# Performance work log

Measured on AMD Instinct MI355X. Metric: run time of the kernel, lower is better.

The kernel has to match this reference:

```python
import jax, jax.numpy as jnp
import numpy as np
from jax import lax

EPS = 1e-6
B, C, F, K = 64, 512, 1024, 3

def rmsnorm2d(x, w):
    # normalize over channel dim (axis=1), learnable per-channel scale
    inv = lax.rsqrt(jnp.mean(x * x, axis=1, keepdims=True) + EPS)
    return x * inv * w[None, :, None, None]

def pointwise(x, W, b):
    # 1x1 conv == per-pixel matmul: [B,C,H,F] x [O,C] -> [B,O,H,F]
    return jnp.einsum('bchf,oc->bohf', x, W) + b[None, :, None, None]

def depthwise_band(x, W, b):
    # depthwise conv, kernel (1,K), same padding along freq axis
    y = lax.conv_general_dilated(
        x, W,
        window_strides=(1, 1),
        padding=((0, 0), (K // 2, K // 2)),
        dimension_numbers=('NCHW', 'OIHW', 'NCHW'),
        feature_group_count=C)
    return y + b[None, :, None, None]

def setup_inputs() -> dict:
    key = jax.random.key(0)
    ks = jax.random.split(key, 6)
    s = 0.02
    return {
        'x_t': jax.random.normal(ks[0], (B, C, 1, F), jnp.float32),
        'h_prev': jax.random.normal(ks[1], (B, C, 1, F), jnp.float32),
        'in_norm_w': jnp.ones((C,), jnp.float32),
        'hid_norm_w': jnp.ones((C,), jnp.float32),
        'out_norm_w': jnp.ones((C,), jnp.float32),
        'xW': jax.random.normal(ks[2], (3 * C, C), jnp.float32) * s,
        'xb': jnp.zeros((3 * C,), jnp.float32),
        'hmixW': jax.random.normal(ks[3], (C, 1, 1, K), jnp.float32) * s,
        'hmixb': jnp.zeros((C,), jnp.float32),
        'hW': jax.random.normal(ks[4], (3 * C, C), jnp.float32) * s,
        'hb': jnp.zeros((3 * C,), jnp.float32),
    }

def reference(x_t, h_prev, in_norm_w, hid_norm_w, out_norm_w,
              xW, xb, hmixW, hmixb, hW, hb):
    xg = pointwise(rmsnorm2d(x_t, in_norm_w), xW, xb)            # [B,3C,1,F]
    hg = pointwise(depthwise_band(rmsnorm2d(h_prev, hid_norm_w), hmixW, hmixb), hW, hb)
    xr, xz, xn = jnp.split(xg, 3, axis=1)
    hr, hz, hn = jnp.split(hg, 3, axis=1)
    reset = jax.nn.sigmoid(xr + hr)
    update = jax.nn.sigmoid(xz + hz)
    cand = jnp.tanh(xn + reset * hn)
    h_new = (1.0 - update) * cand + update * h_prev
    return rmsnorm2d(h_new + x_t, out_norm_w)
```

## Files before the change

### kernel.cpp

```cpp
#include <hip/hip_runtime.h>

typedef __attribute__((ext_vector_type(8))) short short8;
typedef __attribute__((ext_vector_type(4))) float f32x4;
typedef __attribute__((ext_vector_type(4))) unsigned short u16x4;
typedef unsigned short u16;
typedef unsigned int u32;

#define EPSV 1e-6f

__device__ __forceinline__ u16 f2bf(float f){
  u32 u = __float_as_uint(f);
  u = u + 0x7fffu + ((u >> 16) & 1u);
  return (u16)(u >> 16);
}
__device__ __forceinline__ float bf2f(u16 h){
  return __uint_as_float(((u32)h) << 16);
}
__device__ __forceinline__ float sigm(float v){ return 1.f/(1.f + __expf(-v)); }
__device__ __forceinline__ float tanh_fast(float g){
  float e = __expf(-2.f*fabsf(g));
  return copysignf((1.f - e)/(1.f + e), g);
}
__device__ __forceinline__ void gload_lds16(const void* g, void* l){
  __builtin_amdgcn_global_load_lds(
      (const __attribute__((address_space(1))) u32*)g,
      (__attribute__((address_space(3))) u32*)l, 16, 0, 0);
}

#define WS_WXB   0u
#define WS_WHB   1572864u
#define WS_CB    3145728u
#define WS_SSQP  3153920u
#define WS_SBF   7348224u
#define WS_NEED  74457088u

#define GG_SMEM  147456

extern "C" __global__ void wprep(const float* __restrict__ xW, const float* __restrict__ hW,
                                 const float* __restrict__ inw, const float* __restrict__ hidw,
                                 const float* __restrict__ xb, const float* __restrict__ hmixb,
                                 const float* __restrict__ hb,
                                 u16* __restrict__ xWb, u16* __restrict__ hWb,
                                 float* __restrict__ cb){
  __shared__ float red[4];
  const int n = blockIdx.x;
  const int tid = threadIdx.x;
  float pb = 0.f;
  for (int k = tid; k < 512; k += 256){
    float xw = xW[n*512 + k], hw = hW[n*512 + k];
    xWb[n*512 + k] = f2bf(xw * inw[k]);
    hWb[n*512 + k] = f2bf(hw * hidw[k]);
    pb += hw * hmixb[k];
  }
  #pragma unroll
  for (int off = 1; off < 64; off <<= 1) pb += __shfl_xor(pb, off);
  if ((tid & 63) == 0) red[tid >> 6] = pb;
  __syncthreads();
  if (tid == 0){
    float dot = red[0] + red[1] + red[2] + red[3];
    if (n < 1024){ cb[n] = xb[n] + hb[n] + dot; }
    else         { cb[n] = xb[n]; cb[n + 512] = hb[n] + dot; }
  }
}

extern "C" __global__ void __launch_bounds__(256)
wbuild(const float* __restrict__ x, const float* __restrict__ h,
       const float* __restrict__ hmixW,
       u16* __restrict__ Ax, u16* __restrict__ Ahm)
{
  __shared__ float tile[32][264];
  __shared__ float invx_s[256];
  __shared__ float invh_s[258];
  __shared__ float hmw_s[1536];

  const int b = blockIdx.y, fc = blockIdx.x;
  const int f0 = fc*256;
  const int t = threadIdx.x;
  const int r = t >> 3, q = t & 7;

  for (int i = t; i < 1536; i += 256) hmw_s[i] = hmixW[i];

  float ssq = 0.f;
  for (int cc = 0; cc < 16; ++cc){
    __syncthreads();
    const float* src = x + ((size_t)(b*512 + cc*32 + r))*1024 + f0;
    #pragma unroll
    for (int i = 0; i < 8; ++i)
      *(f32x4*)&tile[r][q*4 + i*32] = *(const f32x4*)(src + q*4 + i*32);
    __syncthreads();
    float p = 0.f;
    #pragma unroll
    for (int rr = 0; rr < 32; ++rr){ float v = tile[rr][t]; p += v*v; }
    ssq += p;
  }
  invx_s[t] = rsqrtf(ssq*(1.f/512.f) + EPSV);
  for (int cc = 0; cc < 16; ++cc){
    __syncthreads();
    const float* src = x + ((size_t)(b*512 + cc*32 + r))*1024 + f0;
    #pragma unroll
    for (int i = 0; i < 8; ++i)
      *(f32x4*)&tile[r][q*4 + i*32] = *(const f32x4*)(src + q*4 + i*32);
    __syncthreads();
    #pragma unroll
    for (int it = 0; it < 4; ++it){
      int id = it*256 + t;
      int pix = id >> 2, c8 = (id & 3)*8;
      float iv = invx_s[pix];
      short8 pk;
      #pragma unroll
      for (int j = 0; j < 8; ++j) pk[j] = (short)f2bf(tile[c8+j][pix]*iv);
      *(short8*)(Ax + ((size_t)(b*1024 + f0 + pix))*512 + cc*32 + c8) = pk;
    }
  }
  float ssqh = 0.f, ssqL = 0.f, ssqR = 0.f;
  for (int cc = 0; cc < 16; ++cc){
    __syncthreads();
    const float* src = h + ((size_t)(b*512 + cc*32 + r))*1024 + f0;
    #pragma unroll
    for (int i = 0; i < 8; ++i)
      *(f32x4*)&tile[r][q*4 + i*32] = *(const f32x4*)(src + q*4 + i*32);
    if (t < 32){
      tile[t][256] = (f0 > 0) ? h[((size_t)(b*512 + cc*32 + t))*1024 + f0 - 1] : 0.f;
    } else if (t < 64){
      int rr = t - 32;
      tile[rr][257] = (f0 + 256 < 1024) ? h[((size_t)(b*512 + cc*32 + rr))*1024 + f0 + 256] : 0.f;
    }
    __syncthreads();
    float p = 0.f;
    #pragma unroll
    for (int rr = 0; rr < 32; ++rr){ float v = tile[rr][t]; p += v*v; }
    ssqh += p;
    if (t == 0){ float p2=0.f; for (int rr=0; rr<32; ++rr){ float v=tile[rr][256]; p2+=v*v; } ssqL += p2; }
    if (t == 1){ float p2=0.f; for (int rr=0; rr<32; ++rr){ float v=tile[rr][257]; p2+=v*v; } ssqR += p2; }
  }
  invh_s[1 + t] = rsqrtf(ssqh*(1.f/512.f) + EPSV);
  if (t == 0) invh_s[0]   = rsqrtf(ssqL*(1.f/512.f) + EPSV);
  if (t == 1) invh_s[257] = rsqrtf(ssqR*(1.f/512.f) + EPSV);
  for (int cc = 0; cc < 16; ++cc){
    __syncthreads();
    const float* src = h + ((size_t)(b*512 + cc*32 + r))*1024 + f0;
    #pragma unroll
    for (int i = 0; i < 8; ++i)
      *(f32x4*)&tile[r][q*4 + i*32] = *(const f32x4*)(src + q*4 + i*32);
    if (t < 32){
      tile[t][256] = (f0 > 0) ? h[((size_t)(b*512 + cc*32 + t))*1024 + f0 - 1] : 0.f;
    } else if (t < 64){
      int rr = t - 32;
      tile[rr][257] = (f0 + 256 < 1024) ? h[((size_t)(b*512 + cc*32 + rr))*1024 + f0 + 256] : 0.f;
    }
    __syncthreads();
    #pragma unroll
    for (int it = 0; it < 4; ++it){
      int id = it*256 + t;
      int pix = id >> 2, c8 = (id & 3)*8;
      int colL = (pix == 0)   ? 256 : (pix - 1);
      int colR = (pix == 255) ? 257 : (pix + 1);
      float iL = invh_s[pix], iC = invh_s[pix+1], iR = invh_s[pix+2];
      short8 pk;
      #pragma unroll
      for (int j = 0; j < 8; ++j){
        int c = c8 + j;
        int cg = cc*32 + c;
        float v = hmw_s[cg*3+0]*tile[c][colL]*iL
                + hmw_s[cg*3+1]*tile[c][pix ]*iC
                + hmw_s[cg*3+2]*tile[c][colR]*iR;
        pk[j] = (short)f2bf(v);
      }
      *(short8*)(Ahm + ((size_t)(b*1024 + f0 + pix))*512 + cc*32 + c8) = pk;
    }
  }
}

extern "C" __global__ void __launch_bounds__(256, 1)
gemm_gates(const float* __restrict__ x, const float* __restrict__ h,
           const u16* __restrict__ Abase,
           const u16* __restrict__ xWb, const u16* __restrict__ hWb,
           const float* __restrict__ cb,
           float* __restrict__ ssqp, u16* __restrict__ sbf)
{
  extern __shared__ __align__(16) char smem[];
  const int t = threadIdx.x;
  const int bid = blockIdx.x;
  const int swz = (bid & 7)*512 + (bid >> 3);
  const int mh = swz >> 4, ch = swz & 15;
  const int b = mh >> 2, f0 = (mh & 3)*256;
  const int c0 = ch*32;
  const int pixbase = b*1024 + f0;
  const int w = t >> 6, lane = t & 63, li = lane & 15, lg = lane >> 4;

  char* Bbase = smem + 49152;

  int rrA[4], kqA[4];
  #pragma unroll
  for (int uu = 0; uu < 4; ++uu){
    int u = w*256 + uu*64 + lane;
    rrA[uu] = ((u >> 5) & 7)*8 + (u & 7) + w*64;
    kqA[uu] = (u >> 3) & 3;
  }

  auto stageB = [&](const u16* Wsrc){
    #pragma unroll
    for (int i = 0; i < 24; ++i){
      int fi = i*4 + w;
      int kk = fi / 6, rem = fi - kk*6;
      int g = rem >> 1, ct = rem & 1;
      const u16* src = Wsrc + ((size_t)(g*512 + c0 + ct*16 + li))*512 + kk*32 + lg*8;
      gload_lds16(src, Bbase + fi*1024);
    }
  };
  auto stageA = [&](const u16* Asrc, int kk, int buf){
    char* adst = smem + buf*16384 + w*4096;
    #pragma unroll
    for (int uu = 0; uu < 4; ++uu){
      gload_lds16(Asrc + ((size_t)(pixbase + rrA[uu]))*512 + kk*32 + kqA[uu]*8,
                  adst + uu*1024);
    }
  };

  f32x4 accr[2][4] = {}, accz[2][4] = {}, accg1[2][4] = {}, accg2[2][4] = {};

  auto kstep = [&](int kk, int buf, f32x4 (&accg)[2][4]){
    const char* ab = smem + buf*16384 + w*4096;
    short8 af[4];
    #pragma unroll
    for (int mf = 0; mf < 4; ++mf){
      int rl = mf*16 + li;
      af[mf] = *(const short8*)(ab + ((rl >> 3) << 9) + (lg << 7) + ((rl & 7) << 4));
    }
    #pragma unroll
    for (int ct = 0; ct < 2; ++ct){
      const char* bb = Bbase + (kk*6 + ct)*1024 + lane*16;
      short8 bf0 = *(const short8*)(bb);
      short8 bf1 = *(const short8*)(bb + 2048);
      short8 bf2 = *(const short8*)(bb + 4096);
      #pragma unroll
      for (int mf = 0; mf < 4; ++mf){
        accr[ct][mf] = __builtin_amdgcn_mfma_f32_16x16x32_bf16(af[mf], bf0, accr[ct][mf], 0,0,0);
        accz[ct][mf] = __builtin_amdgcn_mfma_f32_16x16x32_bf16(af[mf], bf1, accz[ct][mf], 0,0,0);
        accg[ct][mf] = __builtin_amdgcn_mfma_f32_16x16x32_bf16(af[mf], bf2, accg[ct][mf], 0,0,0);
      }
    }
  };

  stageB(xWb);
  stageA(Abase, 0, 0);
  stageA(Abase, 1, 1);
  __syncthreads();
  #pragma unroll
  for (int j = 0; j < 16; ++j){
    if (j < 14) stageA(Abase, j + 2, (j + 2) % 3);
    kstep(j, j % 3, accg1);
    if (j < 14)      { asm volatile("s_waitcnt vmcnt(4)" ::: "memory"); }
    else if (j == 14){ asm volatile("s_waitcnt vmcnt(0)" ::: "memory"); }
    __builtin_amdgcn_sched_barrier(0);
  }
  __syncthreads();
  const u16* A1 = Abase + 33554432;
  stageB(hWb);
  stageA(A1, 0, 0);
  stageA(A1, 1, 1);
  __syncthreads();
  #pragma unroll
  for (int j = 0; j < 16; ++j){
    if (j < 14) stageA(A1, j + 2, (j + 2) % 3);
    kstep(j, j % 3, accg2);
    if (j < 14)      { asm volatile("s_waitcnt vmcnt(4)" ::: "memory"); }
    else if (j == 14){ asm volatile("s_waitcnt vmcnt(0)" ::: "memory"); }
    __builtin_amdgcn_sched_barrier(0);
  }
  __syncthreads();

  float (*stg)[264] = (float(*)[264])smem;
  float ps[4][4] = {};
  #pragma unroll
  for (int ct = 0; ct < 2; ++ct){
    const int c = c0 + ct*16 + li;
    const float cbr = cb[c], cbz = cb[512 + c], xbn = cb[1024 + c], hbn = cb[1536 + c];
    #pragma unroll
    for (int mf = 0; mf < 4; ++mf){
      const int f = f0 + w*64 + mf*16 + lg*4;
      const size_t gidx = ((size_t)(b*512 + c))*1024 + f;
      f32x4 hp = *(const f32x4*)(h + gidx);
      f32x4 xt = *(const f32x4*)(x + gidx);
      f32x4 sv;
      #pragma unroll
      for (int j = 0; j < 4; ++j){
        float rr = sigm(accr[ct][mf][j] + cbr);
        float zz = sigm(accz[ct][mf][j] + cbz);
        float g  = accg1[ct][mf][j] + xbn + rr*(accg2[ct][mf][j] + hbn);
        float th = tanh_fast(g);
        float s  = (1.f - zz)*th + zz*hp[j] + xt[j];
        sv[j] = s;
        ps[mf][j] += s*s;
      }
      *(f32x4*)&stg[ct*16 + li][w*64 + mf*16 + lg*4] = sv;
    }
  }
  #pragma unroll
  for (int off = 1; off < 16; off <<= 1)
    #pragma unroll
    for (int mf = 0; mf < 4; ++mf)
      #pragma unroll
      for (int j = 0; j < 4; ++j)
        ps[mf][j] += __shfl_xor(ps[mf][j], off);
  if (li == 0){
    #pragma unroll
    for (int mf = 0; mf < 4; ++mf){
      f32x4 v; v[0]=ps[mf][0]; v[1]=ps[mf][1]; v[2]=ps[mf][2]; v[3]=ps[mf][3];
      *(f32x4*)(ssqp + (size_t)ch*65536 + pixbase + w*64 + mf*16 + lg*4) = v;
    }
  }
  __syncthreads();
  {
    const int cl = t >> 3, seg = t & 7;
    u16* dst = sbf + ((size_t)(b*512 + c0 + cl))*1024 + f0 + seg*32;
    #pragma unroll
    for (int qq = 0; qq < 2; ++qq){
      f32x4 a0 = *(const f32x4*)&stg[cl][seg*32 + qq*16 + 0];
      f32x4 a1 = *(const f32x4*)&stg[cl][seg*32 + qq*16 + 4];
      f32x4 a2 = *(const f32x4*)&stg[cl][seg*32 + qq*16 + 8];
      f32x4 a3 = *(const f32x4*)&stg[cl][seg*32 + qq*16 + 12];
      short8 p0, p1;
      #pragma unroll
      for (int j = 0; j < 4; ++j){
        p0[j]   = (short)f2bf(a0[j]); p0[j+4] = (short)f2bf(a1[j]);
        p1[j]   = (short)f2bf(a2[j]); p1[j+4] = (short)f2bf(a3[j]);
      }
      *(short8*)(dst + qq*16)     = p0;
      *(short8*)(dst + qq*16 + 8) = p1;
    }
  }
}

extern "C" __global__ void __launch_bounds__(256)
outnorm(const float* __restrict__ ssqp, const u16* __restrict__ sbf,
        const float* __restrict__ outw, float* __restrict__ out)
{
  __shared__ float invf[1024];
  const int b = blockIdx.y, cch = blockIdx.x;
  const int t = threadIdx.x;
  f32x4 acc = {};
  #pragma unroll
  for (int p = 0; p < 16; ++p){
    f32x4 v = *(const f32x4*)(ssqp + (size_t)p*65536 + b*1024 + t*4);
    acc[0]+=v[0]; acc[1]+=v[1]; acc[2]+=v[2]; acc[3]+=v[3];
  }
  f32x4 iv;
  #pragma unroll
  for (int j = 0; j < 4; ++j) iv[j] = rsqrtf(acc[j]*(1.f/512.f) + EPSV);
  *(f32x4*)&invf[t*4] = iv;
  __syncthreads();
  for (int cl = 0; cl < 32; ++cl){
    const int c = cch*32 + cl;
    const float ow = outw[c];
    const u16* row = sbf + ((size_t)(b*512 + c))*1024;
    u16x4 sv = *(const u16x4*)(row + t*4);
    f32x4 o;
    #pragma unroll
    for (int j = 0; j < 4; ++j) o[j] = bf2f(sv[j]) * invf[t*4 + j] * ow;
    *(f32x4*)(out + ((size_t)(b*512 + c))*1024 + t*4) = o;
  }
}

#define FB_AXN_OFF 0
#define FB_AHM_OFF 32768
#define FB_RAW_OFF 65536
#define FB_PART_OFF 102400
#define FB_INVX_OFF 104512
#define FB_INVH_OFF 104640
#define FB_SSQ2_OFF 104784
#define FB_INVO_OFF 105936
#define FB_SMEM_BYTES 106112

extern "C" __global__ void fb_wconv(const float* __restrict__ xW, const float* __restrict__ hW,
                                    u16* __restrict__ xWb, u16* __restrict__ hWb){
  int i = blockIdx.x*256 + threadIdx.x;
  xWb[i] = f2bf(xW[i]);
  hWb[i] = f2bf(hW[i]);
}

extern "C" __global__ void __launch_bounds__(512, 2)
fb_gru(const float* __restrict__ x, const float* __restrict__ h,
       const float* __restrict__ inw, const float* __restrict__ hidw,
       const float* __restrict__ outw,
       const float* __restrict__ xb, const float* __restrict__ hmixWc,
       const float* __restrict__ hmixb, const float* __restrict__ hb,
       const u16* __restrict__ xWb, const u16* __restrict__ hWb,
       float* __restrict__ out)
{
  extern __shared__ __align__(16) char smem[];
  const int b  = blockIdx.y;
  const int f0 = blockIdx.x * 32;
  const int t  = threadIdx.x;
  u16* raw = (u16*)(smem + FB_RAW_OFF);
  float* part = (float*)(smem + FB_PART_OFF);
  {
    const int fq = t & 7, cb2 = t >> 3;
    #pragma unroll
    for (int pass = 0; pass < 8; ++pass){
      int c = pass*64 + cb2;
      f32x4 v = *(const f32x4*)(x + ((size_t)(b*512 + c))*1024 + f0 + fq*4);
      u16* d = raw + c*36 + fq*4;
      d[0] = f2bf(v[0]); d[1] = f2bf(v[1]); d[2] = f2bf(v[2]); d[3] = f2bf(v[3]);
    }
  }
  __syncthreads();
  {
    const int f = t & 31, cs = t >> 5;
    float p = 0.f;
    for (int i = 0; i < 32; ++i){ float v = bf2f(raw[(cs*32 + i)*36 + f]); p += v*v; }
    part[cs*33 + f] = p;
  }
  __syncthreads();
  if (t < 32){
    float s = 0.f;
    for (int i = 0; i < 16; ++i) s += part[i*33 + t];
    ((float*)(smem + FB_INVX_OFF))[t] = rsqrtf(s*(1.f/512.f) + EPSV);
  }
  __syncthreads();
  {
    const int f = t >> 4, cc = t & 15;
    const float iv = ((float*)(smem + FB_INVX_OFF))[f];
    #pragma unroll
    for (int it = 0; it < 4; ++it){
      int cbase = (cc + it*16)*8;
      short8 pk;
      #pragma unroll
      for (int j = 0; j < 8; ++j){
        float v = bf2f(raw[(cbase+j)*36 + f]) * iv * inw[cbase+j];
        pk[j] = (short)f2bf(v);
      }
      *(short8*)(smem + FB_AXN_OFF + f*1024 + ((cbase*2) ^ ((f&7)<<4))) = pk;
    }
  }
  __syncthreads();
  {
    const int fq = t & 7, cb2 = t >> 3;
    #pragma unroll
    for (int pass = 0; pass < 8; ++pass){
      int c = pass*64 + cb2;
      f32x4 v = *(const f32x4*)(h + ((size_t)(b*512 + c))*1024 + f0 + fq*4);
      u16* d = raw + c*36 + 1 + fq*4;
      d[0] = f2bf(v[0]); d[1] = f2bf(v[1]); d[2] = f2bf(v[2]); d[3] = f2bf(v[3]);
    }
    {
      int c = t;
      size_t base = ((size_t)(b*512 + c))*1024;
      float lv = (f0 > 0)          ? h[base + f0 - 1]  : 0.f;
      float rv = (f0 + 32 < 1024)  ? h[base + f0 + 32] : 0.f;
      raw[c*36 + 0]  = f2bf(lv);
      raw[c*36 + 33] = f2bf(rv);
    }
  }
  __syncthreads();
  {
    const int fw = t & 63, cs = t >> 6;
    if (fw < 34){
      float p = 0.f;
      for (int i = 0; i < 64; ++i){ float v = bf2f(raw[(cs*64 + i)*36 + fw]); p += v*v; }
      part[cs*35 + fw] = p;
    }
  }
  __syncthreads();
  if (t < 34){
    float s = 0.f;
    for (int i = 0; i < 8; ++i) s += part[i*35 + t];
    ((float*)(smem + FB_INVH_OFF))[t] = rsqrtf(s*(1.f/512.f) + EPSV);
  }
  __syncthreads();
  {
    const int fr = t >> 5, cc = t & 31;
    const float* invh = (const float*)(smem + FB_INVH_OFF);
    const float iL = invh[fr], iC = invh[fr + 1], iR = invh[fr + 2];
    #pragma unroll
    for (int it = 0; it < 2; ++it){
      const int cbase = (cc + it*32)*8;
      short8 o;
      #pragma unroll
      for (int j = 0; j < 8; ++j){
        int c = cbase + j;
        float hL = bf2f(raw[c*36 + fr])     * iL;
        float hC = bf2f(raw[c*36 + fr + 1]) * iC;
        float hR = bf2f(raw[c*36 + fr + 2]) * iR;
        float v = (hmixWc[c*3]*hL + hmixWc[c*3+1]*hC + hmixWc[c*3+2]*hR) * hidw[c] + hmixb[c];
        o[j] = (short)f2bf(v);
      }
      *(short8*)(smem + FB_AHM_OFF + fr*1024 + ((cbase*2) ^ ((fr&7)<<4))) = o;
    }
  }
  __syncthreads();
  const int wv = t >> 6, lane = t & 63, li = lane & 15, lg = lane >> 4;
  const int n0 = wv*64;
  f32x4 ar[2][4] = {}, az[2][4] = {}, axg[2][4] = {}, ahg[2][4] = {};
  #pragma unroll
  for (int src = 0; src < 2; ++src){
    const char* A = smem + (src ? FB_AHM_OFF : FB_AXN_OFF);
    const u16* W = src ? hWb : xWb;
    for (int k0 = 0; k0 < 512; k0 += 32){
      const int kb = (k0*2 + lg*16) ^ ((li & 7) << 4);
      short8 a0 = *(const short8*)(A + li*1024 + kb);
      short8 a1 = *(const short8*)(A + (li+16)*1024 + kb);
      #pragma unroll
      for (int nt = 0; nt < 4; ++nt){
        const u16* bp = W + (size_t)(n0 + nt*16 + li)*512 + k0 + lg*8;
        short8 br = *(const short8*)(bp);
        short8 bz = *(const short8*)(bp + 512*512);
        short8 bg = *(const short8*)(bp + 1024*512);
        ar[0][nt] = __builtin_amdgcn_mfma_f32_16x16x32_bf16(a0, br, ar[0][nt], 0,0,0);
        ar[1][nt] = __builtin_amdgcn_mfma_f32_16x16x32_bf16(a1, br, ar[1][nt], 0,0,0);
        az[0][nt] = __builtin_amdgcn_mfma_f32_16x16x32_bf16(a0, bz, az[0][nt], 0,0,0);
        az[1][nt] = __builtin_amdgcn_mfma_f32_16x16x32_bf16(a1, bz, az[1][nt], 0,0,0);
        if (src == 0){
          axg[0][nt] = __builtin_amdgcn_mfma_f32_16x16x32_bf16(a0, bg, axg[0][nt], 0,0,0);
          axg[1][nt] = __builtin_amdgcn_mfma_f32_16x16x32_bf16(a1, bg, axg[1][nt], 0,0,0);
        } else {
          ahg[0][nt] = __builtin_amdgcn_mfma_f32_16x16x32_bf16(a0, bg, ahg[0][nt], 0,0,0);
          ahg[1][nt] = __builtin_amdgcn_mfma_f32_16x16x32_bf16(a1, bg, ahg[1][nt], 0,0,0);
        }
      }
    }
  }
  float ps[8] = {0,0,0,0,0,0,0,0};
  #pragma unroll
  for (int nt = 0; nt < 4; ++nt){
    const int c = n0 + nt*16 + li;
    const float xbr = xb[c], xbz = xb[512+c], xbg = xb[1024+c];
    const float hbr = hb[c], hbz = hb[512+c], hbg = hb[1024+c];
    #pragma unroll
    for (int mt = 0; mt < 2; ++mt){
      const size_t idx = ((size_t)(b*512 + c))*1024 + f0 + mt*16 + lg*4;
      const f32x4 hp = *(const f32x4*)(h + idx);
      const f32x4 xt = *(const f32x4*)(x + idx);
      f32x4 sv;
      #pragma unroll
      for (int j = 0; j < 4; ++j){
        float rr = sigm(ar[mt][nt][j] + xbr + hbr);
        float zz = sigm(az[mt][nt][j] + xbz + hbz);
        float g  = axg[mt][nt][j] + xbg + rr*(ahg[mt][nt][j] + hbg);
        float th = tanh_fast(g);
        float hv = (1.f - zz)*th + zz*hp[j];
        float s  = hv + xt[j];
        sv[j] = s;
        ps[mt*4 + j] += s*s;
      }
      ar[mt][nt] = sv;
    }
  }
  #pragma unroll
  for (int off = 1; off < 16; off <<= 1){
    #pragma unroll
    for (int p = 0; p < 8; ++p) ps[p] += __shfl_xor(ps[p], off);
  }
  __syncthreads();
  float* stg = (float*)(smem + FB_AXN_OFF);
  #pragma unroll
  for (int nt = 0; nt < 4; ++nt){
    const int n = n0 + nt*16 + li;
    #pragma unroll
    for (int mt = 0; mt < 2; ++mt){
      const int m0 = mt*16 + lg*4;
      *(f32x4*)(stg + n*32 + (m0 ^ ((n & 7) << 2))) = ar[mt][nt];
    }
  }
  float* sq2 = (float*)(smem + FB_SSQ2_OFF);
  if (li == 0){
    #pragma unroll
    for (int p = 0; p < 8; ++p){
      int m = (p >> 2)*16 + lg*4 + (p & 3);
      sq2[m*9 + wv] = ps[p];
    }
  }
  __syncthreads();
  if (t < 32){
    float s = 0.f;
    for (int i = 0; i < 8; ++i) s += sq2[t*9 + i];
    ((float*)(smem + FB_INVO_OFF))[t] = rsqrtf(s*(1.f/512.f) + EPSV);
  }
  __syncthreads();
  {
    const float* invO = (const float*)(smem + FB_INVO_OFF);
    const int cb2 = t >> 3, chh = t & 7;
    #pragma unroll
    for (int pass = 0; pass < 8; ++pass){
      int c = pass*64 + cb2;
      int base = (chh*4) ^ ((c & 7) << 2);
      f32x4 v = *(const f32x4*)(stg + c*32 + base);
      float ow = outw[c];
      f32x4 o;
      #pragma unroll
      for (int j = 0; j < 4; ++j) o[j] = v[j] * invO[chh*4 + j] * ow;
      *(f32x4*)(out + ((size_t)(b*512 + c))*1024 + f0 + chh*4) = o;
    }
  }
}

extern "C" void kernel_launch(void* const* d_in, const int* in_sizes, int n_in,
                              void* d_out, int out_size, void* d_ws, size_t ws_size,
                              hipStream_t stream){
  (void)in_sizes; (void)n_in; (void)out_size;
  const float* x      = (const float*)d_in[0];
  const float* h      = (const float*)d_in[1];
  const float* inw    = (const float*)d_in[2];
  const float* hidw   = (const float*)d_in[3];
  const float* outw   = (const float*)d_in[4];
  const float* xW     = (const float*)d_in[5];
  const float* xb     = (const float*)d_in[6];
  const float* hmixW  = (const float*)d_in[7];
  const float* hmixb  = (const float*)d_in[8];
  const float* hW     = (const float*)d_in[9];
  const float* hb     = (const float*)d_in[10];

  if (ws_size >= (size_t)WS_NEED){
    u16*   xWb  = (u16*)((char*)d_ws + WS_WXB);
    u16*   hWb  = (u16*)((char*)d_ws + WS_WHB);
    float* cbw  = (float*)((char*)d_ws + WS_CB);
    float* ssqp = (float*)((char*)d_ws + WS_SSQP);
    u16*   sbf  = (u16*)((char*)d_ws + WS_SBF);
    u16*   Ax   = (u16*)d_out;

    hipFuncSetAttribute(reinterpret_cast<const void*>(gemm_gates),
                        hipFuncAttributeMaxDynamicSharedMemorySize, GG_SMEM);

    wprep<<<1536, 256, 0, stream>>>(xW, hW, inw, hidw, xb, hmixb, hb, xWb, hWb, cbw);
    wbuild<<<dim3(4, 64), 256, 0, stream>>>(x, h, hmixW, Ax, Ax + 33554432);
    gemm_gates<<<4096, 256, GG_SMEM, stream>>>(x, h, Ax, xWb, hWb, cbw, ssqp, sbf);
    outnorm<<<dim3(16, 64), 256, 0, stream>>>(ssqp, sbf, outw, (float*)d_out);
  } else {
    u16* xWb = (u16*)d_ws;
    u16* hWb = xWb + 786432;
    hipFuncSetAttribute(reinterpret_cast<const void*>(fb_gru),
                        hipFuncAttributeMaxDynamicSharedMemorySize, FB_SMEM_BYTES);
    fb_wconv<<<3072, 256, 0, stream>>>(xW, hW, xWb, hWb);
    dim3 grid(32, 64);
    fb_gru<<<grid, 512, FB_SMEM_BYTES, stream>>>(x, h, inw, hidw, outw,
                                                 xb, hmixW, hmixb, hb,
                                                 xWb, hWb, (float*)d_out);
  }
}
```

Measured before the change: 713.6 us.

## Double gemm_gates pixel tile to 512 with 8 waves and a simplified A layout

```diff
diff --git a/kernel.cpp b/kernel.cpp
--- a/kernel.cpp
+++ b/kernel.cpp
@@ -34,7 +34,7 @@
 #define WS_SBF   7348224u
 #define WS_NEED  74457088u
 
-#define GG_SMEM  147456
+#define GG_SMEM  163840
 
 extern "C" __global__ void wprep(const float* __restrict__ xW, const float* __restrict__ hW,
                                  const float* __restrict__ inw, const float* __restrict__ hidw,
@@ -171,7 +171,7 @@
   }
 }
 
-extern "C" __global__ void __launch_bounds__(256, 1)
+extern "C" __global__ void __launch_bounds__(512, 2)
 gemm_gates(const float* __restrict__ x, const float* __restrict__ h,
            const u16* __restrict__ Abase,
            const u16* __restrict__ xWb, const u16* __restrict__ hWb,
@@ -181,52 +181,42 @@
   extern __shared__ __align__(16) char smem[];
   const int t = threadIdx.x;
   const int bid = blockIdx.x;
-  const int swz = (bid & 7)*512 + (bid >> 3);
+  const int swz = (bid & 7)*256 + (bid >> 3);
   const int mh = swz >> 4, ch = swz & 15;
-  const int b = mh >> 2, f0 = (mh & 3)*256;
+  const int b = mh >> 1, f0 = (mh & 1)*512;
   const int c0 = ch*32;
   const int pixbase = b*1024 + f0;
   const int w = t >> 6, lane = t & 63, li = lane & 15, lg = lane >> 4;
 
-  char* Bbase = smem + 49152;
-
-  int rrA[4], kqA[4];
-  #pragma unroll
-  for (int uu = 0; uu < 4; ++uu){
-    int u = w*256 + uu*64 + lane;
-    rrA[uu] = ((u >> 5) & 7)*8 + (u & 7) + w*64;
-    kqA[uu] = (u >> 3) & 3;
-  }
+  char* Bbase = smem + 65536;
 
   auto stageB = [&](const u16* Wsrc){
     #pragma unroll
-    for (int i = 0; i < 24; ++i){
-      int fi = i*4 + w;
+    for (int i = 0; i < 12; ++i){
+      int fi = i*8 + w;
       int kk = fi / 6, rem = fi - kk*6;
       int g = rem >> 1, ct = rem & 1;
-      const u16* src = Wsrc + ((size_t)(g*512 + c0 + ct*16 + li))*512 + kk*32 + lg*8;
-      gload_lds16(src, Bbase + fi*1024);
+      gload_lds16(Wsrc + ((size_t)(g*512 + c0 + ct*16 + li))*512 + kk*32 + lg*8,
+                  Bbase + fi*1024);
     }
   };
   auto stageA = [&](const u16* Asrc, int kk, int buf){
-    char* adst = smem + buf*16384 + w*4096;
-    #pragma unroll
-    for (int uu = 0; uu < 4; ++uu){
-      gload_lds16(Asrc + ((size_t)(pixbase + rrA[uu]))*512 + kk*32 + kqA[uu]*8,
-                  adst + uu*1024);
+    char* adst = smem + buf*32768 + w*4096;
+    #pragma unroll
+    for (int mf = 0; mf < 4; ++mf){
+      gload_lds16(Asrc + ((size_t)(pixbase + w*64 + mf*16 + li))*512 + kk*32 + lg*8,
+                  adst + mf*1024);
     }
   };
 
   f32x4 accr[2][4] = {}, accz[2][4] = {}, accg1[2][4] = {}, accg2[2][4] = {};
 
   auto kstep = [&](int kk, int buf, f32x4 (&accg)[2][4]){
-    const char* ab = smem + buf*16384 + w*4096;
+    const char* ab = smem + buf*32768 + w*4096;
     short8 af[4];
     #pragma unroll
-    for (int mf = 0; mf < 4; ++mf){
-      int rl = mf*16 + li;
-      af[mf] = *(const short8*)(ab + ((rl >> 3) << 9) + (lg << 7) + ((rl & 7) << 4));
-    }
+    for (int mf = 0; mf < 4; ++mf)
+      af[mf] = *(const short8*)(ab + mf*1024 + lane*16);
     #pragma unroll
     for (int ct = 0; ct < 2; ++ct){
       const char* bb = Bbase + (kk*6 + ct)*1024 + lane*16;
@@ -244,33 +234,29 @@
 
   stageB(xWb);
   stageA(Abase, 0, 0);
-  stageA(Abase, 1, 1);
   __syncthreads();
   #pragma unroll
   for (int j = 0; j < 16; ++j){
-    if (j < 14) stageA(Abase, j + 2, (j + 2) % 3);
-    kstep(j, j % 3, accg1);
-    if (j < 14)      { asm volatile("s_waitcnt vmcnt(4)" ::: "memory"); }
-    else if (j == 14){ asm volatile("s_waitcnt vmcnt(0)" ::: "memory"); }
+    if (j < 15) stageA(Abase, j + 1, (j + 1) & 1);
+    kstep(j, j & 1, accg1);
+    if (j < 15){ asm volatile("s_waitcnt vmcnt(0)" ::: "memory"); }
     __builtin_amdgcn_sched_barrier(0);
   }
   __syncthreads();
   const u16* A1 = Abase + 33554432;
   stageB(hWb);
   stageA(A1, 0, 0);
-  stageA(A1, 1, 1);
   __syncthreads();
   #pragma unroll
   for (int j = 0; j < 16; ++j){
-    if (j < 14) stageA(A1, j + 2, (j + 2) % 3);
-    kstep(j, j % 3, accg2);
-    if (j < 14)      { asm volatile("s_waitcnt vmcnt(4)" ::: "memory"); }
-    else if (j == 14){ asm volatile("s_waitcnt vmcnt(0)" ::: "memory"); }
+    if (j < 15) stageA(A1, j + 1, (j + 1) & 1);
+    kstep(j, j & 1, accg2);
+    if (j < 15){ asm volatile("s_waitcnt vmcnt(0)" ::: "memory"); }
     __builtin_amdgcn_sched_barrier(0);
   }
   __syncthreads();
 
-  float (*stg)[264] = (float(*)[264])smem;
+  float (*stg)[516] = (float(*)[516])smem;
   float ps[4][4] = {};
   #pragma unroll
   for (int ct = 0; ct < 2; ++ct){
@@ -312,7 +298,7 @@
   }
   __syncthreads();
   {
-    const int cl = t >> 3, seg = t & 7;
+    const int cl = t >> 4, seg = t & 15;
     u16* dst = sbf + ((size_t)(b*512 + c0 + cl))*1024 + f0 + seg*32;
     #pragma unroll
     for (int qq = 0; qq < 2; ++qq){
@@ -623,7 +609,7 @@
 
     wprep<<<1536, 256, 0, stream>>>(xW, hW, inw, hidw, xb, hmixb, hb, xWb, hWb, cbw);
     wbuild<<<dim3(4, 64), 256, 0, stream>>>(x, h, hmixW, Ax, Ax + 33554432);
-    gemm_gates<<<4096, 256, GG_SMEM, stream>>>(x, h, Ax, xWb, hWb, cbw, ssqp, sbf);
+    gemm_gates<<<2048, 512, GG_SMEM, stream>>>(x, h, Ax, xWb, hWb, cbw, ssqp, sbf);
     outnorm<<<dim3(16, 64), 256, 0, stream>>>(ssqp, sbf, outw, (float*)d_out);
   } else {
     u16* xWb = (u16*)d_ws;
```

After: 614.5 us. 13.9% less time.
